# Kernel optimization log

Hardware: AMD Instinct MI355X
Metric: run time of the kernel (lower is better)

The kernel has to match this reference:

```python
import jax, jax.numpy as jnp
import numpy as np

T = 3072          # num tokens
HID = 5120        # hidden_size
H = 16            # num_local_heads
DN = 128          # qk_nope_head_dim
DR = 64           # qk_rope_head_dim
DQK = DN + DR     # qk_head_dim = 192
DV = 128          # v_head_dim
Q_RANK = 1536     # q_lora_rank
KV_RANK = 512     # kv_lora_rank


def rmsnorm(x, w, eps=1e-6):
    var = jnp.mean(jnp.square(x), axis=-1, keepdims=True)
    return x * jax.lax.rsqrt(var + eps) * w


def apply_rope(x, cos, sin):
    # neox-style rotate-half; x [..., DR], cos/sin broadcastable [..., DR//2]
    x1, x2 = jnp.split(x, 2, axis=-1)
    return jnp.concatenate([x1 * cos - x2 * sin, x2 * cos + x1 * sin], axis=-1)


def setup_inputs() -> dict:
    key = jax.random.key(0)
    ks = jax.random.split(key, 8)
    s = 0.02
    positions = jnp.arange(T, dtype=jnp.int32)
    hidden_states = jax.random.normal(ks[0], (T, HID), dtype=jnp.float32)
    llama_4_scaling = jnp.ones((T, 1, 1), dtype=jnp.float32)
    w_q_a = jax.random.normal(ks[1], (HID, Q_RANK), dtype=jnp.float32) * s
    q_a_ln_w = jnp.ones((Q_RANK,), dtype=jnp.float32)
    w_q_b = jax.random.normal(ks[2], (Q_RANK, H * DQK), dtype=jnp.float32) * s
    w_kv_a = jax.random.normal(ks[3], (HID, KV_RANK + DR), dtype=jnp.float32) * s
    kv_a_ln_w = jnp.ones((KV_RANK,), dtype=jnp.float32)
    w_kv_b = jax.random.normal(ks[4], (KV_RANK, H * (DN + DV)), dtype=jnp.float32) * s
    w_o = jax.random.normal(ks[5], (H * DV, HID), dtype=jnp.float32) * s
    # cos/sin cache: [max_pos, DR]; first half cos, second half sin
    inv_freq = 1.0 / (10000.0 ** (jnp.arange(0, DR, 2, dtype=jnp.float32) / DR))
    t = jnp.arange(T, dtype=jnp.float32)
    freqs = t[:, None] * inv_freq[None, :]              # [T, DR//2]
    cos_sin_cache = jnp.concatenate([jnp.cos(freqs), jnp.sin(freqs)], axis=-1)
    return {
        "positions": positions, "hidden_states": hidden_states,
        "llama_4_scaling": llama_4_scaling,
        "w_q_a": w_q_a, "q_a_ln_w": q_a_ln_w, "w_q_b": w_q_b,
        "w_kv_a": w_kv_a, "kv_a_ln_w": kv_a_ln_w, "w_kv_b": w_kv_b,
        "w_o": w_o, "cos_sin_cache": cos_sin_cache,
    }


def reference(positions, hidden_states, llama_4_scaling, w_q_a, q_a_ln_w,
              w_q_b, w_kv_a, kv_a_ln_w, w_kv_b, w_o, cos_sin_cache):
    # ---- Q path: low-rank down/up projection with RMSNorm ----
    q = rmsnorm(hidden_states @ w_q_a, q_a_ln_w) @ w_q_b       # [T, H*DQK]
    q = q.reshape(T, H, DQK)
    q_nope, q_pe = q[..., :DN], q[..., DN:]                    # [T,H,DN],[T,H,DR]

    # ---- KV path: compressed latent + shared rope key ----
    latent = hidden_states @ w_kv_a                            # [T, KV_RANK+DR]
    kv_a = rmsnorm(latent[:, :KV_RANK], kv_a_ln_w)             # [T, KV_RANK]
    k_pe = latent[:, KV_RANK:]                                 # [T, DR] (shared across heads)
    kv = (kv_a @ w_kv_b).reshape(T, H, DN + DV)
    k_nope, v = kv[..., :DN], kv[..., DN:]                     # [T,H,DN],[T,H,DV]

    # ---- partial RoPE on the rope slices only ----
    cs = cos_sin_cache[positions]                              # [T, DR]
    cos, sin = cs[:, :DR // 2], cs[:, DR // 2:]
    q_pe = apply_rope(q_pe, cos[:, None, :], sin[:, None, :])
    k_pe = apply_rope(k_pe, cos, sin)

    q = jnp.concatenate([q_nope, q_pe], axis=-1)               # [T, H, DQK]
    k = jnp.concatenate(
        [k_nope, jnp.broadcast_to(k_pe[:, None, :], (T, H, DR))], axis=-1)

    q = q * llama_4_scaling

    # ---- causal attention (v is zero-padded to DQK in the original;
    #      the pad contributes zeros and is sliced off, so we skip it) ----
    scale = 1.0 / jnp.sqrt(jnp.float32(DQK))
    scores = jnp.einsum('qhd,khd->hqk', q, k) * scale          # [H, T, T]
    causal = positions[:, None] >= positions[None, :]
    scores = jnp.where(causal[None, :, :], scores, jnp.finfo(scores.dtype).min)
    probs = jax.nn.softmax(scores, axis=-1)
    attn = jnp.einsum('hqk,khd->qhd', probs, v)                # [T, H, DV]

    return attn.reshape(T, H * DV) @ w_o                       # [T, HID]
```

## Files before the change

kernel.cpp:

```cpp
#include <hip/hip_runtime.h>
#include <hip/hip_bf16.h>
#include <math.h>

#define T_TOK 3072
#define HID_D 5120
#define NH 16
#define DN 128
#define DR 64
#define DQK 192
#define DV 128
#define QRANK 1536
#define KVRANK 512

typedef __attribute__((ext_vector_type(8))) short short8;
typedef __attribute__((ext_vector_type(4))) float f32x4;
typedef unsigned short u16;

__device__ __forceinline__ u16 f2bf(float f) {
    unsigned int u = __float_as_uint(f);
    unsigned int lsb = (u >> 16) & 1;
    u += 0x7fffu + lsb;
    return (u16)(u >> 16);
}

__device__ __forceinline__ void gload_lds16(const u16* g, u16* l) {
    __builtin_amdgcn_global_load_lds((const __attribute__((address_space(1))) void*)g,
                                     (__attribute__((address_space(3))) void*)l, 16, 0, 0);
}

__global__ __launch_bounds__(256) void convert_bf_k(const float* __restrict__ x,
                                                    u16* __restrict__ y, int n4)
{
    const int i = blockIdx.x * 256 + threadIdx.x;
    if (i < n4) {
        float4 v = ((const float4*)x)[i];
        ushort4 o;
        o.x = f2bf(v.x); o.y = f2bf(v.y); o.z = f2bf(v.z); o.w = f2bf(v.w);
        ((ushort4*)y)[i] = o;
    }
}

__global__ __launch_bounds__(256) void transpose_conv_k(const float* __restrict__ W,
                                                        u16* __restrict__ WT,
                                                        int K, int N)
{
    __shared__ float tile[32][33];
    const int n0 = blockIdx.x * 32, k0 = blockIdx.y * 32;
    const int tx = threadIdx.x & 31, ty = threadIdx.x >> 5;
#pragma unroll
    for (int i = 0; i < 32; i += 8) {
        const int nn = n0 + tx;
        tile[ty + i][tx] = (nn < N) ? W[(size_t)(k0 + ty + i) * N + nn] : 0.f;
    }
    __syncthreads();
#pragma unroll
    for (int i = 0; i < 32; i += 8) {
        WT[(size_t)(n0 + ty + i) * K + k0 + tx] = f2bf(tile[tx][ty + i]);
    }
}

template <bool BF16_OUT>
__global__ __launch_bounds__(256) void bgemm_bt_k(
    const u16* __restrict__ A, const u16* __restrict__ BT, void* __restrict__ C,
    int Nreal, int K, int lda, int ldb, int ldc)
{
    __shared__ __attribute__((aligned(16))) u16 As[128 * 32];
    __shared__ __attribute__((aligned(16))) u16 Bs[128 * 32];

    const int tid  = threadIdx.x;
    const int wave = tid >> 6, lane = tid & 63;
    const int quad = lane >> 4, l16 = lane & 15;
    const int wr = (wave >> 1) * 64, wc = (wave & 1) * 64;
    const int row0 = blockIdx.y * 128, col0 = blockIdx.x * 128;

    f32x4 acc[4][4];
#pragma unroll
    for (int i = 0; i < 4; ++i)
#pragma unroll
        for (int j = 0; j < 4; ++j) acc[i][j] = (f32x4){0.f, 0.f, 0.f, 0.f};

    const int sr  = tid >> 2;
    const int skc = (tid & 3) * 8;
    const u16* ap0 = A  + (size_t)(row0 + sr)      * lda + skc;
    const u16* ap1 = A  + (size_t)(row0 + sr + 64) * lda + skc;
    const u16* bp0 = BT + (size_t)(col0 + sr)      * ldb + skc;
    const u16* bp1 = BT + (size_t)(col0 + sr + 64) * ldb + skc;
    u16* al0 = As + tid * 8;
    u16* al1 = As + tid * 8 + 64 * 32;
    u16* bl0 = Bs + tid * 8;
    u16* bl1 = Bs + tid * 8 + 64 * 32;

    for (int kt = 0; kt < K; kt += 32) {
        gload_lds16(ap0 + kt, al0);
        gload_lds16(ap1 + kt, al1);
        gload_lds16(bp0 + kt, bl0);
        gload_lds16(bp1 + kt, bl1);
        __syncthreads();

        short8 af[4], bf[4];
#pragma unroll
        for (int mi = 0; mi < 4; ++mi)
            af[mi] = *(const short8*)(As + (wr + mi * 16 + l16) * 32 + quad * 8);
#pragma unroll
        for (int ni = 0; ni < 4; ++ni)
            bf[ni] = *(const short8*)(Bs + (wc + ni * 16 + l16) * 32 + quad * 8);
#pragma unroll
        for (int mi = 0; mi < 4; ++mi)
#pragma unroll
            for (int ni = 0; ni < 4; ++ni)
                acc[mi][ni] = __builtin_amdgcn_mfma_f32_16x16x32_bf16(
                    af[mi], bf[ni], acc[mi][ni], 0, 0, 0);
        __syncthreads();
    }

#pragma unroll
    for (int mi = 0; mi < 4; ++mi) {
#pragma unroll
        for (int ni = 0; ni < 4; ++ni) {
            const int col_g = col0 + wc + ni * 16 + l16;
            if (col_g < Nreal) {
#pragma unroll
                for (int r = 0; r < 4; ++r) {
                    const int row_g = row0 + wr + mi * 16 + quad * 4 + r;
                    if (BF16_OUT)
                        ((u16*)C)[(size_t)row_g * ldc + col_g] = f2bf(acc[mi][ni][r]);
                    else
                        ((float*)C)[(size_t)row_g * ldc + col_g] = acc[mi][ni][r];
                }
            }
        }
    }
}

__global__ __launch_bounds__(256) void rmsnorm_conv_k(const float* __restrict__ x,
                                                      const float* __restrict__ w,
                                                      u16* __restrict__ y,
                                                      int width, int stride)
{
    const int row = blockIdx.x;
    const float* xr = x + (size_t)row * stride;
    float ss = 0.f;
    for (int i = threadIdx.x; i < width; i += 256) {
        float v = xr[i];
        ss += v * v;
    }
    __shared__ float red[256];
    red[threadIdx.x] = ss;
    __syncthreads();
    for (int s = 128; s > 0; s >>= 1) {
        if (threadIdx.x < s) red[threadIdx.x] += red[threadIdx.x + s];
        __syncthreads();
    }
    const float scale = rsqrtf(red[0] / (float)width + 1e-6f);
    for (int i = threadIdx.x; i < width; i += 256)
        y[(size_t)row * width + i] = f2bf(xr[i] * scale * w[i]);
}

__global__ void rope_scale_q_conv_k(const float* __restrict__ q, const int* __restrict__ positions,
                                    const float* __restrict__ scaling,
                                    const float* __restrict__ cs_cache, u16* __restrict__ qb)
{
    const int t = blockIdx.x;
    const int pos = positions[t];
    const float* cs = cs_cache + (size_t)pos * DR;
    const float s = scaling[t];
    __shared__ float c_sh[32], s_sh[32];
    if (threadIdx.x < 32) {
        c_sh[threadIdx.x] = cs[threadIdx.x];
        s_sh[threadIdx.x] = cs[32 + threadIdx.x];
    }
    __syncthreads();
    const int tid = threadIdx.x;
    for (int h = 0; h < NH; ++h) {
        const float* qr = q + ((size_t)t * NH + h) * DQK;
        u16* qo = qb + ((size_t)t * NH + h) * DQK;
        if (tid < 128) {
            qo[tid] = f2bf(qr[tid] * s);
        } else if (tid < 160) {
            const int d = tid - 128;
            const float x1 = qr[128 + d], x2 = qr[160 + d];
            qo[128 + d] = f2bf((x1 * c_sh[d] - x2 * s_sh[d]) * s);
            qo[160 + d] = f2bf((x2 * c_sh[d] + x1 * s_sh[d]) * s);
        }
    }
}

__global__ void rope_k_conv_k(const float* __restrict__ latent, u16* __restrict__ kpe,
                              const int* __restrict__ positions,
                              const float* __restrict__ cs_cache)
{
    const int t = blockIdx.x;
    const int d = threadIdx.x;
    if (d >= 32) return;
    const int pos = positions[t];
    const float* cs = cs_cache + (size_t)pos * DR;
    const float c = cs[d], sn = cs[32 + d];
    const float* lr = latent + (size_t)t * (KVRANK + DR) + KVRANK;
    const float x1 = lr[d], x2 = lr[32 + d];
    kpe[(size_t)t * DR + d]      = f2bf(x1 * c - x2 * sn);
    kpe[(size_t)t * DR + 32 + d] = f2bf(x2 * c + x1 * sn);
}

#define ATT_BM 64
#define ATT_BN 64
__global__ __launch_bounds__(256) void attn_mfma_k(
    const u16* __restrict__ qb, const u16* __restrict__ kvb,
    const u16* __restrict__ kpeb, u16* __restrict__ attnb)
{
    __shared__ u16 Ks[ATT_BN][200];
    __shared__ u16 Vt[DV][72];
    __shared__ u16 Ps[4][16][72];

    const int tid  = threadIdx.x;
    const int wave = tid >> 6;
    const int lane = tid & 63;
    const int quad = lane >> 4;
    const int l16  = lane & 15;

    const int qblk = blockIdx.x;
    const int h    = blockIdx.y;
    const int q0   = qblk * ATT_BM;
    const int qrow = q0 + wave * 16 + l16;

    short8 qf[6];
    {
        const u16* qp = qb + ((size_t)qrow * NH + h) * DQK + quad * 8;
#pragma unroll
        for (int c = 0; c < 6; ++c)
            qf[c] = *(const short8*)(qp + c * 32);
    }

    f32x4 oacc[8];
#pragma unroll
    for (int t = 0; t < 8; ++t) oacc[t] = (f32x4){0.f, 0.f, 0.f, 0.f};
    float m_old[4], l_run[4];
#pragma unroll
    for (int r = 0; r < 4; ++r) { m_old[r] = -1e30f; l_run[r] = 0.f; }

    const int nkt = qblk + 1;
    for (int kt = 0; kt < nkt; ++kt) {
        const int k0 = kt * ATT_BN;
        __syncthreads();
        for (int cc = tid; cc < 64 * 24; cc += 256) {
            const int row = cc / 24, c = cc % 24;
            short8 v;
            if (c < 16) v = *(const short8*)(kvb + ((size_t)(k0 + row) * NH + h) * (DN + DV) + c * 8);
            else        v = *(const short8*)(kpeb + (size_t)(k0 + row) * DR + (c - 16) * 8);
            *(short8*)&Ks[row][c * 8] = v;
        }
        {
            const int j  = tid & 63;
            const int db = (tid >> 6) * 32;
            const u16* src = kvb + ((size_t)(k0 + j) * NH + h) * (DN + DV) + DN + db;
#pragma unroll
            for (int i = 0; i < 32; i += 4) {
                ushort4 v4 = *(const ushort4*)(src + i);
                Vt[db + i + 0][j] = v4.x;
                Vt[db + i + 1][j] = v4.y;
                Vt[db + i + 2][j] = v4.z;
                Vt[db + i + 3][j] = v4.w;
            }
        }
        __syncthreads();

        f32x4 sacc[4];
#pragma unroll
        for (int t = 0; t < 4; ++t) sacc[t] = (f32x4){0.f, 0.f, 0.f, 0.f};
#pragma unroll
        for (int t = 0; t < 4; ++t) {
            const u16* kp = &Ks[t * 16 + l16][quad * 8];
#pragma unroll
            for (int c = 0; c < 6; ++c) {
                short8 bfrag = *(const short8*)(kp + c * 32);
                sacc[t] = __builtin_amdgcn_mfma_f32_16x16x32_bf16(qf[c], bfrag, sacc[t], 0, 0, 0);
            }
        }
        const float sc = 0.07216878364870322f;
        const int rbase = q0 + wave * 16 + quad * 4;
#pragma unroll
        for (int t = 0; t < 4; ++t) {
            const int colg = k0 + t * 16 + l16;
#pragma unroll
            for (int r = 0; r < 4; ++r) {
                const float s = sacc[t][r] * sc;
                sacc[t][r] = (rbase + r >= colg) ? s : -1e30f;
            }
        }
        float alpha[4];
#pragma unroll
        for (int r = 0; r < 4; ++r) {
            float mx = fmaxf(fmaxf(sacc[0][r], sacc[1][r]), fmaxf(sacc[2][r], sacc[3][r]));
            mx = fmaxf(mx, __shfl_xor(mx, 1));
            mx = fmaxf(mx, __shfl_xor(mx, 2));
            mx = fmaxf(mx, __shfl_xor(mx, 4));
            mx = fmaxf(mx, __shfl_xor(mx, 8));
            const float mnew = fmaxf(m_old[r], mx);
            alpha[r] = __expf(m_old[r] - mnew);
            float sum = 0.f;
#pragma unroll
            for (int t = 0; t < 4; ++t) {
                const float p = __expf(sacc[t][r] - mnew);
                sacc[t][r] = p;
                sum += p;
            }
            sum += __shfl_xor(sum, 1);
            sum += __shfl_xor(sum, 2);
            sum += __shfl_xor(sum, 4);
            sum += __shfl_xor(sum, 8);
            l_run[r] = l_run[r] * alpha[r] + sum;
            m_old[r] = mnew;
        }
#pragma unroll
        for (int t = 0; t < 4; ++t)
#pragma unroll
            for (int r = 0; r < 4; ++r)
                Ps[wave][quad * 4 + r][t * 16 + l16] = f2bf(sacc[t][r]);
#pragma unroll
        for (int t = 0; t < 8; ++t)
#pragma unroll
            for (int r = 0; r < 4; ++r)
                oacc[t][r] *= alpha[r];
        __syncthreads();

#pragma unroll
        for (int ch = 0; ch < 2; ++ch) {
            short8 pfrag = *(const short8*)&Ps[wave][l16][ch * 32 + quad * 8];
#pragma unroll
            for (int t = 0; t < 8; ++t) {
                short8 vfrag = *(const short8*)&Vt[t * 16 + l16][ch * 32 + quad * 8];
                oacc[t] = __builtin_amdgcn_mfma_f32_16x16x32_bf16(pfrag, vfrag, oacc[t], 0, 0, 0);
            }
        }
    }

#pragma unroll
    for (int r = 0; r < 4; ++r) {
        const float linv = 1.f / l_run[r];
        const int row_g = q0 + wave * 16 + quad * 4 + r;
        u16* op = attnb + (size_t)row_g * (NH * DV) + h * DV;
#pragma unroll
        for (int t = 0; t < 8; ++t)
            op[t * 16 + l16] = f2bf(oacc[t][r] * linv);
    }
}

extern "C" void kernel_launch(void* const* d_in, const int* in_sizes, int n_in,
                              void* d_out, int out_size, void* d_ws, size_t ws_size,
                              hipStream_t stream)
{
    const int*   positions = (const int*)d_in[0];
    const float* hidden    = (const float*)d_in[1];
    const float* scaling   = (const float*)d_in[2];
    const float* w_q_a     = (const float*)d_in[3];
    const float* q_a_ln_w  = (const float*)d_in[4];
    const float* w_q_b     = (const float*)d_in[5];
    const float* w_kv_a    = (const float*)d_in[6];
    const float* kv_a_ln_w = (const float*)d_in[7];
    const float* w_kv_b    = (const float*)d_in[8];
    const float* w_o       = (const float*)d_in[9];
    const float* cs_cache  = (const float*)d_in[10];
    float* out = (float*)d_out;

    char* p = (char*)d_ws;
    auto alloc = [&](size_t bytes) { char* r = p; p += (bytes + 255) & ~(size_t)255; return r; };

    char* regA      = alloc((size_t)T_TOK * NH * DQK * 4);
    u16*  hidden_bf = (u16*)regA;
    float* qbuf     = (float*)regA;
    char* regB    = alloc((size_t)T_TOK * QRANK * 4);
    float* q_a    = (float*)regB;
    u16*  qb      = (u16*)regB;
    float* latent = (float*)alloc((size_t)T_TOK * (KVRANK + DR) * 4);
    u16* kpe_bf   = (u16*)alloc((size_t)T_TOK * DR * 2);
    u16* kv_bf    = (u16*)alloc((size_t)T_TOK * NH * (DN + DV) * 2);
    u16* attnb    = (u16*)alloc((size_t)T_TOK * NH * DV * 2);
    u16* q_a_bf   = (u16*)alloc((size_t)T_TOK * QRANK * 2);
    u16* kv_a_bf  = (u16*)alloc((size_t)T_TOK * KVRANK * 2);
    u16* wqa_bt   = (u16*)alloc((size_t)QRANK * HID_D * 2);
    u16* wkva_bt  = (u16*)alloc((size_t)640 * HID_D * 2);
    u16* wqb_bt   = (u16*)alloc((size_t)(NH * DQK) * QRANK * 2);
    u16* wkvb_bt  = (u16*)alloc((size_t)(NH * (DN + DV)) * KVRANK * 2);
    u16* wo_bt    = (u16*)alloc((size_t)HID_D * (NH * DV) * 2);

    const dim3 blk(256);

    convert_bf_k<<<dim3((T_TOK * HID_D / 4 + 255) / 256), blk, 0, stream>>>(
        hidden, hidden_bf, T_TOK * HID_D / 4);
    transpose_conv_k<<<dim3(QRANK / 32, HID_D / 32), blk, 0, stream>>>(w_q_a, wqa_bt, HID_D, QRANK);
    transpose_conv_k<<<dim3(640 / 32, HID_D / 32), blk, 0, stream>>>(w_kv_a, wkva_bt, HID_D, KVRANK + DR);
    transpose_conv_k<<<dim3(NH * DQK / 32, QRANK / 32), blk, 0, stream>>>(w_q_b, wqb_bt, QRANK, NH * DQK);
    transpose_conv_k<<<dim3(NH * (DN + DV) / 32, KVRANK / 32), blk, 0, stream>>>(w_kv_b, wkvb_bt, KVRANK, NH * (DN + DV));
    transpose_conv_k<<<dim3(HID_D / 32, NH * DV / 32), blk, 0, stream>>>(w_o, wo_bt, NH * DV, HID_D);

    bgemm_bt_k<false><<<dim3(QRANK / 128, T_TOK / 128), blk, 0, stream>>>(
        hidden_bf, wqa_bt, q_a, QRANK, HID_D, HID_D, HID_D, QRANK);
    bgemm_bt_k<false><<<dim3(640 / 128, T_TOK / 128), blk, 0, stream>>>(
        hidden_bf, wkva_bt, latent, KVRANK + DR, HID_D, HID_D, HID_D, KVRANK + DR);
    rope_k_conv_k<<<dim3(T_TOK), dim3(64), 0, stream>>>(latent, kpe_bf, positions, cs_cache);
    rmsnorm_conv_k<<<dim3(T_TOK), blk, 0, stream>>>(q_a, q_a_ln_w, q_a_bf, QRANK, QRANK);
    rmsnorm_conv_k<<<dim3(T_TOK), blk, 0, stream>>>(latent, kv_a_ln_w, kv_a_bf, KVRANK, KVRANK + DR);
    bgemm_bt_k<false><<<dim3(NH * DQK / 128, T_TOK / 128), blk, 0, stream>>>(
        q_a_bf, wqb_bt, qbuf, NH * DQK, QRANK, QRANK, QRANK, NH * DQK);
    rope_scale_q_conv_k<<<dim3(T_TOK), blk, 0, stream>>>(qbuf, positions, scaling, cs_cache, qb);
    bgemm_bt_k<true><<<dim3(NH * (DN + DV) / 128, T_TOK / 128), blk, 0, stream>>>(
        kv_a_bf, wkvb_bt, kv_bf, NH * (DN + DV), KVRANK, KVRANK, KVRANK, NH * (DN + DV));
    attn_mfma_k<<<dim3(T_TOK / ATT_BM, NH), blk, 0, stream>>>(qb, kv_bf, kpe_bf, attnb);
    bgemm_bt_k<false><<<dim3(HID_D / 128, T_TOK / 128), blk, 0, stream>>>(
        attnb, wo_bt, out, HID_D, NH * DV, NH * DV, NH * DV, HID_D);
}
```

Baseline: 925.5 us.

## Merge q_a/kv_a GEMMs, emit bf16 intermediates, pre-transpose V, enlarge attention tiles

Fuses the w_q_a and w_kv_a projections into one GEMM over a concatenated 2176-wide weight, and makes the intermediate GEMMs write bf16 instead of fp32, so the rmsnorm and rope kernels read half the bytes. V is transposed once by a new kernel rather than scattered into shared memory inside every attention tile. The attention kernel moves to 128-row query blocks with 512 threads, launches the heaviest causal blocks first, and lets waves skip fully masked key tiles. It also drops one barrier. Rounding intermediates to bf16 adds precision error, and the bigger blocks change occupancy.

After: 802.9 us. -13.2%, faster.

```diff
diff --git a/kernel.cpp b/kernel.cpp
--- a/kernel.cpp
+++ b/kernel.cpp
@@ -11,6 +11,7 @@
 #define DV 128
 #define QRANK 1536
 #define KVRANK 512
+#define MERGED_N 2176
 
 typedef __attribute__((ext_vector_type(8))) short short8;
 typedef __attribute__((ext_vector_type(4))) float f32x4;
@@ -21,6 +22,9 @@
     unsigned int lsb = (u >> 16) & 1;
     u += 0x7fffu + lsb;
     return (u16)(u >> 16);
+}
+__device__ __forceinline__ float bf2f(u16 v) {
+    return __uint_as_float(((unsigned int)v) << 16);
 }
 
 __device__ __forceinline__ void gload_lds16(const u16* g, u16* l) {
@@ -132,16 +136,16 @@
     }
 }
 
-__global__ __launch_bounds__(256) void rmsnorm_conv_k(const float* __restrict__ x,
-                                                      const float* __restrict__ w,
-                                                      u16* __restrict__ y,
-                                                      int width, int stride)
+__global__ __launch_bounds__(256) void rmsnorm_bf_k(const u16* __restrict__ x,
+                                                    const float* __restrict__ w,
+                                                    u16* __restrict__ y,
+                                                    int width, int stride, int off)
 {
     const int row = blockIdx.x;
-    const float* xr = x + (size_t)row * stride;
+    const u16* xr = x + (size_t)row * stride + off;
     float ss = 0.f;
     for (int i = threadIdx.x; i < width; i += 256) {
-        float v = xr[i];
+        float v = bf2f(xr[i]);
         ss += v * v;
     }
     __shared__ float red[256];
@@ -153,12 +157,12 @@
     }
     const float scale = rsqrtf(red[0] / (float)width + 1e-6f);
     for (int i = threadIdx.x; i < width; i += 256)
-        y[(size_t)row * width + i] = f2bf(xr[i] * scale * w[i]);
-}
-
-__global__ void rope_scale_q_conv_k(const float* __restrict__ q, const int* __restrict__ positions,
-                                    const float* __restrict__ scaling,
-                                    const float* __restrict__ cs_cache, u16* __restrict__ qb)
+        y[(size_t)row * width + i] = f2bf(bf2f(xr[i]) * scale * w[i]);
+}
+
+__global__ void rope_scale_q_bf_k(const u16* __restrict__ q, const int* __restrict__ positions,
+                                  const float* __restrict__ scaling,
+                                  const float* __restrict__ cs_cache, u16* __restrict__ qb)
 {
     const int t = blockIdx.x;
     const int pos = positions[t];
@@ -172,22 +176,22 @@
     __syncthreads();
     const int tid = threadIdx.x;
     for (int h = 0; h < NH; ++h) {
-        const float* qr = q + ((size_t)t * NH + h) * DQK;
+        const u16* qr = q + ((size_t)t * NH + h) * DQK;
         u16* qo = qb + ((size_t)t * NH + h) * DQK;
         if (tid < 128) {
-            qo[tid] = f2bf(qr[tid] * s);
+            qo[tid] = f2bf(bf2f(qr[tid]) * s);
         } else if (tid < 160) {
             const int d = tid - 128;
-            const float x1 = qr[128 + d], x2 = qr[160 + d];
+            const float x1 = bf2f(qr[128 + d]), x2 = bf2f(qr[160 + d]);
             qo[128 + d] = f2bf((x1 * c_sh[d] - x2 * s_sh[d]) * s);
             qo[160 + d] = f2bf((x2 * c_sh[d] + x1 * s_sh[d]) * s);
         }
     }
 }
 
-__global__ void rope_k_conv_k(const float* __restrict__ latent, u16* __restrict__ kpe,
-                              const int* __restrict__ positions,
-                              const float* __restrict__ cs_cache)
+__global__ void rope_k_bf_k(const u16* __restrict__ qa_lat, u16* __restrict__ kpe,
+                            const int* __restrict__ positions,
+                            const float* __restrict__ cs_cache)
 {
     const int t = blockIdx.x;
     const int d = threadIdx.x;
@@ -195,21 +199,43 @@
     const int pos = positions[t];
     const float* cs = cs_cache + (size_t)pos * DR;
     const float c = cs[d], sn = cs[32 + d];
-    const float* lr = latent + (size_t)t * (KVRANK + DR) + KVRANK;
-    const float x1 = lr[d], x2 = lr[32 + d];
+    const u16* lr = qa_lat + (size_t)t * MERGED_N + QRANK + KVRANK;
+    const float x1 = bf2f(lr[d]), x2 = bf2f(lr[32 + d]);
     kpe[(size_t)t * DR + d]      = f2bf(x1 * c - x2 * sn);
     kpe[(size_t)t * DR + 32 + d] = f2bf(x2 * c + x1 * sn);
 }
 
-#define ATT_BM 64
+__global__ __launch_bounds__(256) void transpose_v_k(const u16* __restrict__ kvb,
+                                                     u16* __restrict__ vt)
+{
+    __shared__ u16 tile[64][72];
+    const int t0 = blockIdx.x * 64, d0 = blockIdx.y * 64, h = blockIdx.z;
+    const int tid = threadIdx.x;
+    for (int cc = tid; cc < 64 * 8; cc += 256) {
+        const int row = cc >> 3, c = (cc & 7) * 8;
+        *(short8*)&tile[row][c] =
+            *(const short8*)(kvb + ((size_t)(t0 + row) * NH + h) * (DN + DV) + DN + d0 + c);
+    }
+    __syncthreads();
+    for (int cc = tid; cc < 64 * 8; cc += 256) {
+        const int drow = cc >> 3, c = (cc & 7) * 8;
+        short8 s;
+#pragma unroll
+        for (int j = 0; j < 8; ++j) s[j] = tile[c + j][drow];
+        *(short8*)(vt + ((size_t)h * DV + d0 + drow) * T_TOK + t0 + c) = s;
+    }
+}
+
+#define ATT_BM 128
 #define ATT_BN 64
-__global__ __launch_bounds__(256) void attn_mfma_k(
+__global__ __launch_bounds__(512) void attn_mfma_k(
     const u16* __restrict__ qb, const u16* __restrict__ kvb,
-    const u16* __restrict__ kpeb, u16* __restrict__ attnb)
+    const u16* __restrict__ kpeb, const u16* __restrict__ vt,
+    u16* __restrict__ attnb)
 {
     __shared__ u16 Ks[ATT_BN][200];
     __shared__ u16 Vt[DV][72];
-    __shared__ u16 Ps[4][16][72];
+    __shared__ u16 Ps[8][16][72];
 
     const int tid  = threadIdx.x;
     const int wave = tid >> 6;
@@ -217,10 +243,11 @@
     const int quad = lane >> 4;
     const int l16  = lane & 15;
 
-    const int qblk = blockIdx.x;
+    const int qblk = (int)gridDim.x - 1 - (int)blockIdx.x;
     const int h    = blockIdx.y;
     const int q0   = qblk * ATT_BM;
-    const int qrow = q0 + wave * 16 + l16;
+    const int wrow0 = q0 + wave * 16;
+    const int qrow  = wrow0 + l16;
 
     short8 qf[6];
     {
@@ -237,106 +264,105 @@
 #pragma unroll
     for (int r = 0; r < 4; ++r) { m_old[r] = -1e30f; l_run[r] = 0.f; }
 
-    const int nkt = qblk + 1;
+    const int nkt = (q0 + ATT_BM) / ATT_BN;
     for (int kt = 0; kt < nkt; ++kt) {
         const int k0 = kt * ATT_BN;
         __syncthreads();
-        for (int cc = tid; cc < 64 * 24; cc += 256) {
+        for (int cc = tid; cc < 64 * 24; cc += 512) {
             const int row = cc / 24, c = cc % 24;
             short8 v;
             if (c < 16) v = *(const short8*)(kvb + ((size_t)(k0 + row) * NH + h) * (DN + DV) + c * 8);
             else        v = *(const short8*)(kpeb + (size_t)(k0 + row) * DR + (c - 16) * 8);
             *(short8*)&Ks[row][c * 8] = v;
         }
-        {
-            const int j  = tid & 63;
-            const int db = (tid >> 6) * 32;
-            const u16* src = kvb + ((size_t)(k0 + j) * NH + h) * (DN + DV) + DN + db;
-#pragma unroll
-            for (int i = 0; i < 32; i += 4) {
-                ushort4 v4 = *(const ushort4*)(src + i);
-                Vt[db + i + 0][j] = v4.x;
-                Vt[db + i + 1][j] = v4.y;
-                Vt[db + i + 2][j] = v4.z;
-                Vt[db + i + 3][j] = v4.w;
+        for (int cc = tid; cc < DV * 8; cc += 512) {
+            const int row = cc >> 3, c = (cc & 7) * 8;
+            *(short8*)&Vt[row][c] =
+                *(const short8*)(vt + ((size_t)h * DV + row) * T_TOK + k0 + c);
+        }
+        __syncthreads();
+
+        if (k0 <= wrow0 + 15) {
+            f32x4 sacc[4];
+#pragma unroll
+            for (int t = 0; t < 4; ++t) sacc[t] = (f32x4){0.f, 0.f, 0.f, 0.f};
+#pragma unroll
+            for (int t = 0; t < 4; ++t) {
+                const u16* kp = &Ks[t * 16 + l16][quad * 8];
+#pragma unroll
+                for (int c = 0; c < 6; ++c) {
+                    short8 bfrag = *(const short8*)(kp + c * 32);
+                    sacc[t] = __builtin_amdgcn_mfma_f32_16x16x32_bf16(qf[c], bfrag, sacc[t], 0, 0, 0);
+                }
+            }
+            const float sc = 0.07216878364870322f;
+            const int rbase = wrow0 + quad * 4;
+            if (k0 + ATT_BN - 1 > wrow0) {
+#pragma unroll
+                for (int t = 0; t < 4; ++t) {
+                    const int colg = k0 + t * 16 + l16;
+#pragma unroll
+                    for (int r = 0; r < 4; ++r) {
+                        const float s = sacc[t][r] * sc;
+                        sacc[t][r] = (rbase + r >= colg) ? s : -1e30f;
+                    }
+                }
+            } else {
+#pragma unroll
+                for (int t = 0; t < 4; ++t)
+#pragma unroll
+                    for (int r = 0; r < 4; ++r) sacc[t][r] *= sc;
+            }
+            float alpha[4];
+#pragma unroll
+            for (int r = 0; r < 4; ++r) {
+                float mx = fmaxf(fmaxf(sacc[0][r], sacc[1][r]), fmaxf(sacc[2][r], sacc[3][r]));
+                mx = fmaxf(mx, __shfl_xor(mx, 1));
+                mx = fmaxf(mx, __shfl_xor(mx, 2));
+                mx = fmaxf(mx, __shfl_xor(mx, 4));
+                mx = fmaxf(mx, __shfl_xor(mx, 8));
+                const float mnew = fmaxf(m_old[r], mx);
+                alpha[r] = __expf(m_old[r] - mnew);
+                float sum = 0.f;
+#pragma unroll
+                for (int t = 0; t < 4; ++t) {
+                    const float p = __expf(sacc[t][r] - mnew);
+                    sacc[t][r] = p;
+                    sum += p;
+                }
+                sum += __shfl_xor(sum, 1);
+                sum += __shfl_xor(sum, 2);
+                sum += __shfl_xor(sum, 4);
+                sum += __shfl_xor(sum, 8);
+                l_run[r] = l_run[r] * alpha[r] + sum;
+                m_old[r] = mnew;
+            }
+#pragma unroll
+            for (int t = 0; t < 4; ++t)
+#pragma unroll
+                for (int r = 0; r < 4; ++r)
+                    Ps[wave][quad * 4 + r][t * 16 + l16] = f2bf(sacc[t][r]);
+#pragma unroll
+            for (int t = 0; t < 8; ++t)
+#pragma unroll
+                for (int r = 0; r < 4; ++r)
+                    oacc[t][r] *= alpha[r];
+#pragma unroll
+            for (int ch = 0; ch < 2; ++ch) {
+                short8 pfrag = *(const short8*)&Ps[wave][l16][ch * 32 + quad * 8];
+#pragma unroll
+                for (int t = 0; t < 8; ++t) {
+                    short8 vfrag = *(const short8*)&Vt[t * 16 + l16][ch * 32 + quad * 8];
+                    oacc[t] = __builtin_amdgcn_mfma_f32_16x16x32_bf16(pfrag, vfrag, oacc[t], 0, 0, 0);
+                }
             }
         }
-        __syncthreads();
-
-        f32x4 sacc[4];
-#pragma unroll
-        for (int t = 0; t < 4; ++t) sacc[t] = (f32x4){0.f, 0.f, 0.f, 0.f};
-#pragma unroll
-        for (int t = 0; t < 4; ++t) {
-            const u16* kp = &Ks[t * 16 + l16][quad * 8];
-#pragma unroll
-            for (int c = 0; c < 6; ++c) {
-                short8 bfrag = *(const short8*)(kp + c * 32);
-                sacc[t] = __builtin_amdgcn_mfma_f32_16x16x32_bf16(qf[c], bfrag, sacc[t], 0, 0, 0);
-            }
-        }
-        const float sc = 0.07216878364870322f;
-        const int rbase = q0 + wave * 16 + quad * 4;
-#pragma unroll
-        for (int t = 0; t < 4; ++t) {
-            const int colg = k0 + t * 16 + l16;
-#pragma unroll
-            for (int r = 0; r < 4; ++r) {
-                const float s = sacc[t][r] * sc;
-                sacc[t][r] = (rbase + r >= colg) ? s : -1e30f;
-            }
-        }
-        float alpha[4];
-#pragma unroll
-        for (int r = 0; r < 4; ++r) {
-            float mx = fmaxf(fmaxf(sacc[0][r], sacc[1][r]), fmaxf(sacc[2][r], sacc[3][r]));
-            mx = fmaxf(mx, __shfl_xor(mx, 1));
-            mx = fmaxf(mx, __shfl_xor(mx, 2));
-            mx = fmaxf(mx, __shfl_xor(mx, 4));
-            mx = fmaxf(mx, __shfl_xor(mx, 8));
-            const float mnew = fmaxf(m_old[r], mx);
-            alpha[r] = __expf(m_old[r] - mnew);
-            float sum = 0.f;
-#pragma unroll
-            for (int t = 0; t < 4; ++t) {
-                const float p = __expf(sacc[t][r] - mnew);
-                sacc[t][r] = p;
-                sum += p;
-            }
-            sum += __shfl_xor(sum, 1);
-            sum += __shfl_xor(sum, 2);
-            sum += __shfl_xor(sum, 4);
-            sum += __shfl_xor(sum, 8);
-            l_run[r] = l_run[r] * alpha[r] + sum;
-            m_old[r] = mnew;
-        }
-#pragma unroll
-        for (int t = 0; t < 4; ++t)
-#pragma unroll
-            for (int r = 0; r < 4; ++r)
-                Ps[wave][quad * 4 + r][t * 16 + l16] = f2bf(sacc[t][r]);
-#pragma unroll
-        for (int t = 0; t < 8; ++t)
-#pragma unroll
-            for (int r = 0; r < 4; ++r)
-                oacc[t][r] *= alpha[r];
-        __syncthreads();
-
-#pragma unroll
-        for (int ch = 0; ch < 2; ++ch) {
-            short8 pfrag = *(const short8*)&Ps[wave][l16][ch * 32 + quad * 8];
-#pragma unroll
-            for (int t = 0; t < 8; ++t) {
-                short8 vfrag = *(const short8*)&Vt[t * 16 + l16][ch * 32 + quad * 8];
-                oacc[t] = __builtin_amdgcn_mfma_f32_16x16x32_bf16(pfrag, vfrag, oacc[t], 0, 0, 0);
-            }
-        }
     }
 
 #pragma unroll
     for (int r = 0; r < 4; ++r) {
         const float linv = 1.f / l_run[r];
-        const int row_g = q0 + wave * 16 + quad * 4 + r;
+        const int row_g = wrow0 + quad * 4 + r;
         u16* op = attnb + (size_t)row_g * (NH * DV) + h * DV;
 #pragma unroll
         for (int t = 0; t < 8; ++t)
@@ -364,47 +390,47 @@
     char* p = (char*)d_ws;
     auto alloc = [&](size_t bytes) { char* r = p; p += (bytes + 255) & ~(size_t)255; return r; };
 
-    char* regA      = alloc((size_t)T_TOK * NH * DQK * 4);
-    u16*  hidden_bf = (u16*)regA;
-    float* qbuf     = (float*)regA;
-    char* regB    = alloc((size_t)T_TOK * QRANK * 4);
-    float* q_a    = (float*)regB;
-    u16*  qb      = (u16*)regB;
-    float* latent = (float*)alloc((size_t)T_TOK * (KVRANK + DR) * 4);
-    u16* kpe_bf   = (u16*)alloc((size_t)T_TOK * DR * 2);
-    u16* kv_bf    = (u16*)alloc((size_t)T_TOK * NH * (DN + DV) * 2);
-    u16* attnb    = (u16*)alloc((size_t)T_TOK * NH * DV * 2);
-    u16* q_a_bf   = (u16*)alloc((size_t)T_TOK * QRANK * 2);
-    u16* kv_a_bf  = (u16*)alloc((size_t)T_TOK * KVRANK * 2);
-    u16* wqa_bt   = (u16*)alloc((size_t)QRANK * HID_D * 2);
-    u16* wkva_bt  = (u16*)alloc((size_t)640 * HID_D * 2);
-    u16* wqb_bt   = (u16*)alloc((size_t)(NH * DQK) * QRANK * 2);
-    u16* wkvb_bt  = (u16*)alloc((size_t)(NH * (DN + DV)) * KVRANK * 2);
-    u16* wo_bt    = (u16*)alloc((size_t)HID_D * (NH * DV) * 2);
+    char* regH      = alloc((size_t)T_TOK * HID_D * 2);
+    u16*  hidden_bf = (u16*)regH;
+    u16*  qraw_bf   = (u16*)regH;
+    char* regQ      = alloc((size_t)T_TOK * MERGED_N * 2 + (size_t)T_TOK * QRANK * 2);
+    u16*  qa_lat    = (u16*)regQ;
+    u16*  q_a_norm  = (u16*)(regQ + (size_t)T_TOK * MERGED_N * 2);
+    u16*  qb        = (u16*)regQ;
+    u16* kv_a_norm = (u16*)alloc((size_t)T_TOK * KVRANK * 2);
+    u16* kpe_bf    = (u16*)alloc((size_t)T_TOK * DR * 2);
+    u16* kv_bf     = (u16*)alloc((size_t)T_TOK * NH * (DN + DV) * 2);
+    u16* vt        = (u16*)alloc((size_t)NH * DV * T_TOK * 2);
+    u16* attnb     = (u16*)alloc((size_t)T_TOK * NH * DV * 2);
+    u16* wqakva_bt = (u16*)alloc((size_t)MERGED_N * HID_D * 2);
+    u16* wqb_bt    = (u16*)alloc((size_t)(NH * DQK) * QRANK * 2);
+    u16* wkvb_bt   = (u16*)alloc((size_t)(NH * (DN + DV)) * KVRANK * 2);
+    u16* wo_bt     = (u16*)alloc((size_t)HID_D * (NH * DV) * 2);
 
     const dim3 blk(256);
 
     convert_bf_k<<<dim3((T_TOK * HID_D / 4 + 255) / 256), blk, 0, stream>>>(
         hidden, hidden_bf, T_TOK * HID_D / 4);
-    transpose_conv_k<<<dim3(QRANK / 32, HID_D / 32), blk, 0, stream>>>(w_q_a, wqa_bt, HID_D, QRANK);
-    transpose_conv_k<<<dim3(640 / 32, HID_D / 32), blk, 0, stream>>>(w_kv_a, wkva_bt, HID_D, KVRANK + DR);
+    transpose_conv_k<<<dim3(QRANK / 32, HID_D / 32), blk, 0, stream>>>(
+        w_q_a, wqakva_bt, HID_D, QRANK);
+    transpose_conv_k<<<dim3(640 / 32, HID_D / 32), blk, 0, stream>>>(
+        w_kv_a, wqakva_bt + (size_t)QRANK * HID_D, HID_D, KVRANK + DR);
     transpose_conv_k<<<dim3(NH * DQK / 32, QRANK / 32), blk, 0, stream>>>(w_q_b, wqb_bt, QRANK, NH * DQK);
     transpose_conv_k<<<dim3(NH * (DN + DV) / 32, KVRANK / 32), blk, 0, stream>>>(w_kv_b, wkvb_bt, KVRANK, NH * (DN + DV));
     transpose_conv_k<<<dim3(HID_D / 32, NH * DV / 32), blk, 0, stream>>>(w_o, wo_bt, NH * DV, HID_D);
 
-    bgemm_bt_k<false><<<dim3(QRANK / 128, T_TOK / 128), blk, 0, stream>>>(
-        hidden_bf, wqa_bt, q_a, QRANK, HID_D, HID_D, HID_D, QRANK);
-    bgemm_bt_k<false><<<dim3(640 / 128, T_TOK / 128), blk, 0, stream>>>(
-        hidden_bf, wkva_bt, latent, KVRANK + DR, HID_D, HID_D, HID_D, KVRANK + DR);
-    rope_k_conv_k<<<dim3(T_TOK), dim3(64), 0, stream>>>(latent, kpe_bf, positions, cs_cache);
-    rmsnorm_conv_k<<<dim3(T_TOK), blk, 0, stream>>>(q_a, q_a_ln_w, q_a_bf, QRANK, QRANK);
-    rmsnorm_conv_k<<<dim3(T_TOK), blk, 0, stream>>>(latent, kv_a_ln_w, kv_a_bf, KVRANK, KVRANK + DR);
-    bgemm_bt_k<false><<<dim3(NH * DQK / 128, T_TOK / 128), blk, 0, stream>>>(
-        q_a_bf, wqb_bt, qbuf, NH * DQK, QRANK, QRANK, QRANK, NH * DQK);
-    rope_scale_q_conv_k<<<dim3(T_TOK), blk, 0, stream>>>(qbuf, positions, scaling, cs_cache, qb);
+    bgemm_bt_k<true><<<dim3(MERGED_N / 128, T_TOK / 128), blk, 0, stream>>>(
+        hidden_bf, wqakva_bt, qa_lat, QRANK + KVRANK + DR, HID_D, HID_D, HID_D, MERGED_N);
+    rope_k_bf_k<<<dim3(T_TOK), dim3(64), 0, stream>>>(qa_lat, kpe_bf, positions, cs_cache);
+    rmsnorm_bf_k<<<dim3(T_TOK), blk, 0, stream>>>(qa_lat, q_a_ln_w, q_a_norm, QRANK, MERGED_N, 0);
+    rmsnorm_bf_k<<<dim3(T_TOK), blk, 0, stream>>>(qa_lat, kv_a_ln_w, kv_a_norm, KVRANK, MERGED_N, QRANK);
+    bgemm_bt_k<true><<<dim3(NH * DQK / 128, T_TOK / 128), blk, 0, stream>>>(
+        q_a_norm, wqb_bt, qraw_bf, NH * DQK, QRANK, QRANK, QRANK, NH * DQK);
+    rope_scale_q_bf_k<<<dim3(T_TOK), blk, 0, stream>>>(qraw_bf, positions, scaling, cs_cache, qb);
     bgemm_bt_k<true><<<dim3(NH * (DN + DV) / 128, T_TOK / 128), blk, 0, stream>>>(
-        kv_a_bf, wkvb_bt, kv_bf, NH * (DN + DV), KVRANK, KVRANK, KVRANK, NH * (DN + DV));
-    attn_mfma_k<<<dim3(T_TOK / ATT_BM, NH), blk, 0, stream>>>(qb, kv_bf, kpe_bf, attnb);
+        kv_a_norm, wkvb_bt, kv_bf, NH * (DN + DV), KVRANK, KVRANK, KVRANK, NH * (DN + DV));
+    transpose_v_k<<<dim3(T_TOK / 64, DV / 64, NH), blk, 0, stream>>>(kv_bf, vt);
+    attn_mfma_k<<<dim3(T_TOK / ATT_BM, NH), dim3(512), 0, stream>>>(qb, kv_bf, kpe_bf, vt, attnb);
     bgemm_bt_k<false><<<dim3(HID_D / 128, T_TOK / 128), blk, 0, stream>>>(
         attnb, wo_bt, out, HID_D, NH * DV, NH * DV, NH * DV, HID_D);
 }
```
